# Kernel optimization log

Measured on AMD Instinct MI355X. Metric: run time of the kernel, lower is better.

The kernel has to match this reference:

```python
import jax, jax.numpy as jnp
import numpy as np

HIDDEN = 2048
N_HEADS = 16
N_KV = 4
HEAD_DIM = 128
EPS = 1e-6
B = 8
L = 1024
PREFIX = 256
SUFFIX = L - PREFIX
N_COMPACT = PREFIX + B * SUFFIX  # 6400
T_FULL = B * L                   # 8192
ROPE_THETA = 10000.0


def _radix_indices():
    # full position (b, p) -> compact index
    scatter = np.empty(T_FULL, dtype=np.int64)
    for b in range(B):
        scatter[b * L: b * L + PREFIX] = np.arange(PREFIX)
        scatter[b * L + PREFIX: (b + 1) * L] = PREFIX + b * SUFFIX + np.arange(SUFFIX)
    # compact index -> first full occurrence
    fold = np.empty(N_COMPACT, dtype=np.int64)
    fold[:PREFIX] = np.arange(PREFIX)
    for b in range(B):
        fold[PREFIX + b * SUFFIX: PREFIX + (b + 1) * SUFFIX] = b * L + PREFIX + np.arange(SUFFIX)
    return scatter, fold


def setup_inputs() -> dict:
    key = jax.random.key(0)
    ks = jax.random.split(key, 8)
    scatter_np, fold_np = _radix_indices()
    # per-compact-token positions for RoPE
    pos = np.empty(N_COMPACT, dtype=np.float32)
    pos[:PREFIX] = np.arange(PREFIX)
    for b in range(B):
        pos[PREFIX + b * SUFFIX: PREFIX + (b + 1) * SUFFIX] = PREFIX + np.arange(SUFFIX)
    inv_freq = ROPE_THETA ** (-np.arange(HEAD_DIM // 2, dtype=np.float32) / (HEAD_DIM // 2))
    freqs = pos[:, None] * inv_freq[None, :]  # [N_c, 64]
    s = 0.02
    return {
        "hidden_states": jax.random.normal(ks[0], (N_COMPACT, HIDDEN), jnp.float32),
        "cos": jnp.asarray(np.cos(freqs), jnp.float32),
        "sin": jnp.asarray(np.sin(freqs), jnp.float32),
        "cu_seq_lengths": jnp.arange(B + 1, dtype=jnp.int32) * L,
        "max_seq_len": L,
        "fold_gather": jnp.asarray(fold_np),
        "scatter_indices": jnp.asarray(scatter_np),
        "wq": jax.random.normal(ks[1], (HIDDEN, N_HEADS * HEAD_DIM), jnp.float32) * s,
        "wk": jax.random.normal(ks[2], (HIDDEN, N_KV * HEAD_DIM), jnp.float32) * s,
        "wv": jax.random.normal(ks[3], (HIDDEN, N_KV * HEAD_DIM), jnp.float32) * s,
        "wo": jax.random.normal(ks[4], (N_HEADS * HEAD_DIM, HIDDEN), jnp.float32) * s,
        "q_norm_w": jnp.ones((HEAD_DIM,), jnp.float32),
        "k_norm_w": jnp.ones((HEAD_DIM,), jnp.float32),
    }


def _rmsnorm(x, w):
    xf = x.astype(jnp.float32)
    var = jnp.mean(xf * xf, axis=-1, keepdims=True)
    return (w * (xf * jax.lax.rsqrt(var + EPS))).astype(x.dtype)


def _rope(x, cos, sin):
    # x: [N, H, D]; cos/sin: [N, D/2]
    half = cos.shape[-1]
    x1, x2 = x[..., :half], x[..., half:2 * half]
    c, s = cos[:, None, :], sin[:, None, :]
    return jnp.concatenate([x1 * c - x2 * s, x1 * s + x2 * c], axis=-1)


def reference(hidden_states, cos, sin, cu_seq_lengths, max_seq_len,
              fold_gather, scatter_indices, wq, wk, wv, wo, q_norm_w, k_norm_w):
    N = hidden_states.shape[0]
    q = (hidden_states @ wq).reshape(N, N_HEADS, HEAD_DIM)
    k = (hidden_states @ wk).reshape(N, N_KV, HEAD_DIM)
    v = (hidden_states @ wv).reshape(N, N_KV, HEAD_DIM)
    q = _rope(_rmsnorm(q, q_norm_w), cos, sin)
    k = _rope(_rmsnorm(k, k_norm_w), cos, sin)
    # radix scatter: expand compact tokens to full varlen token stream
    qf = q[scatter_indices].reshape(B, L, N_HEADS, HEAD_DIM)
    kf = k[scatter_indices].reshape(B, L, N_KV, HEAD_DIM)
    vf = v[scatter_indices].reshape(B, L, N_KV, HEAD_DIM)
    group = N_HEADS // N_KV
    kf = jnp.repeat(kf, group, axis=2)
    vf = jnp.repeat(vf, group, axis=2)
    scale = HEAD_DIM ** -0.5
    scores = jnp.einsum('bqhd,bkhd->bhqk', qf, kf) * scale
    causal = jnp.tril(jnp.ones((L, L), dtype=bool))
    scores = jnp.where(causal[None, None], scores, jnp.finfo(scores.dtype).min)
    probs = jax.nn.softmax(scores, axis=-1)
    out = jnp.einsum('bhqk,bkhd->bqhd', probs, vf).reshape(T_FULL, N_HEADS * HEAD_DIM)
    # radix fold: gather back to compact tokens
    out_compact = out[fold_gather]
    return out_compact @ wo
```

## Files before the change

### kernel.cpp

```cpp
#include <hip/hip_runtime.h>
#include <hip/hip_bf16.h>

typedef __bf16 bf16;
typedef __bf16 bf16x8 __attribute__((ext_vector_type(8)));
typedef float f32x4 __attribute__((ext_vector_type(4)));

#define HID 2048
#define NHEADS 16
#define NKV 4
#define HD 128
#define NC 6400
#define KVW (NKV * HD)

__device__ __forceinline__ void async_cp16(const bf16* src, bf16* dst_lds) {
  __builtin_amdgcn_global_load_lds(
      (const __attribute__((address_space(1))) void*)src,
      (__attribute__((address_space(3))) void*)dst_lds, 16, 0, 0);
}

__global__ __launch_bounds__(256) void k_cvt(const float* __restrict__ in,
                                             bf16* __restrict__ out) {
  size_t i = ((size_t)blockIdx.x * 256 + threadIdx.x) * 8;
  f32x4 a = *(const f32x4*)(in + i);
  f32x4 b = *(const f32x4*)(in + i + 4);
  bf16x8 t;
  for (int j = 0; j < 4; j++) {
    t[j] = (bf16)a[j];
    t[j + 4] = (bf16)b[j];
  }
  *(bf16x8*)(out + i) = t;
}

__global__ __launch_bounds__(256) void k_transpose(const float* __restrict__ in,
                                                   bf16* __restrict__ out,
                                                   int R, int C) {
  __shared__ bf16 tile[32][33];
  int bc = blockIdx.x * 32, br = blockIdx.y * 32;
  int tx = threadIdx.x & 31, ty = threadIdx.x >> 5;
  for (int i = 0; i < 32; i += 8)
    tile[ty + i][tx] = (bf16)in[(size_t)(br + ty + i) * C + bc + tx];
  __syncthreads();
  for (int i = 0; i < 32; i += 8)
    out[(size_t)(bc + ty + i) * R + br + tx] = tile[tx][ty + i];
}

__global__ __launch_bounds__(256) void k_proj(const bf16* __restrict__ A,
                                              const bf16* __restrict__ wqT,
                                              const bf16* __restrict__ wkT,
                                              const bf16* __restrict__ wvT,
                                              bf16* __restrict__ qb,
                                              bf16* __restrict__ kb,
                                              bf16* __restrict__ vtb) {
  __shared__ __align__(16) bf16 As[128][32];
  __shared__ __align__(16) bf16 Bs[128][32];
  const int K = HID;
  int n0 = blockIdx.x * 128, m0 = blockIdx.y * 128;
  int tid = threadIdx.x;
  int lane = tid & 63, wave = tid >> 6;
  int wm = (wave >> 1) * 64, wn = (wave & 1) * 64;
  int l15 = lane & 15, quad = lane >> 4;

  const bf16* bt;
  int nloc, outsel;
  if (n0 < HID) {
    bt = wqT; nloc = n0; outsel = 0;
  } else if (n0 < HID + KVW) {
    bt = wkT; nloc = n0 - HID; outsel = 1;
  } else {
    bt = wvT; nloc = n0 - HID - KVW; outsel = 2;
  }

  const f32x4 fz = {0.0f, 0.0f, 0.0f, 0.0f};
  f32x4 acc[4][4];
  for (int i = 0; i < 4; i++)
    for (int j = 0; j < 4; j++) acc[i][j] = fz;

  for (int k0 = 0; k0 < K; k0 += 32) {
    for (int s = 0; s < 2; s++) {
      int c = s * 256 + tid;
      int row = c >> 2, kc = c & 3;
      bf16* lbase = &As[0][0] + (size_t)(s * 256 + wave * 64) * 8;
      async_cp16(A + (size_t)(m0 + row) * K + k0 + kc * 8, lbase);
      bf16* lbase2 = &Bs[0][0] + (size_t)(s * 256 + wave * 64) * 8;
      async_cp16(bt + (size_t)(nloc + row) * K + k0 + kc * 8, lbase2);
    }
    __syncthreads();
    bf16x8 af[4], bfr[4];
    for (int t = 0; t < 4; t++) {
      af[t] = *(const bf16x8*)&As[wm + t * 16 + l15][quad * 8];
      bfr[t] = *(const bf16x8*)&Bs[wn + t * 16 + l15][quad * 8];
    }
    for (int i = 0; i < 4; i++)
      for (int j = 0; j < 4; j++)
        acc[i][j] =
            __builtin_amdgcn_mfma_f32_16x16x32_bf16(af[i], bfr[j], acc[i][j], 0, 0, 0);
    __syncthreads();
  }
  for (int i = 0; i < 4; i++)
    for (int j = 0; j < 4; j++)
      for (int r = 0; r < 4; r++) {
        int row = m0 + wm + i * 16 + quad * 4 + r;
        int col = nloc + wn + j * 16 + l15;
        float v = acc[i][j][r];
        if (outsel == 0)
          qb[(size_t)row * HID + col] = (bf16)v;
        else if (outsel == 1)
          kb[(size_t)row * KVW + col] = (bf16)v;
        else
          vtb[(size_t)col * NC + row] = (bf16)v;
      }
}

__global__ __launch_bounds__(256) void k_gemm_out(const bf16* __restrict__ A,
                                                  const bf16* __restrict__ Bt,
                                                  float* __restrict__ C,
                                                  int M, int N, int K) {
  __shared__ __align__(16) bf16 As[128][32];
  __shared__ __align__(16) bf16 Bs[128][32];
  int n0 = blockIdx.x * 128, m0 = blockIdx.y * 128;
  int tid = threadIdx.x;
  int lane = tid & 63, wave = tid >> 6;
  int wm = (wave >> 1) * 64, wn = (wave & 1) * 64;
  int l15 = lane & 15, quad = lane >> 4;

  const f32x4 fz = {0.0f, 0.0f, 0.0f, 0.0f};
  f32x4 acc[4][4];
  for (int i = 0; i < 4; i++)
    for (int j = 0; j < 4; j++) acc[i][j] = fz;

  for (int k0 = 0; k0 < K; k0 += 32) {
    for (int s = 0; s < 2; s++) {
      int c = s * 256 + tid;
      int row = c >> 2, kc = c & 3;
      bf16* lbase = &As[0][0] + (size_t)(s * 256 + wave * 64) * 8;
      async_cp16(A + (size_t)(m0 + row) * K + k0 + kc * 8, lbase);
      bf16* lbase2 = &Bs[0][0] + (size_t)(s * 256 + wave * 64) * 8;
      async_cp16(Bt + (size_t)(n0 + row) * K + k0 + kc * 8, lbase2);
    }
    __syncthreads();
    bf16x8 af[4], bfr[4];
    for (int t = 0; t < 4; t++) {
      af[t] = *(const bf16x8*)&As[wm + t * 16 + l15][quad * 8];
      bfr[t] = *(const bf16x8*)&Bs[wn + t * 16 + l15][quad * 8];
    }
    for (int i = 0; i < 4; i++)
      for (int j = 0; j < 4; j++)
        acc[i][j] =
            __builtin_amdgcn_mfma_f32_16x16x32_bf16(af[i], bfr[j], acc[i][j], 0, 0, 0);
    __syncthreads();
  }
  for (int i = 0; i < 4; i++)
    for (int j = 0; j < 4; j++)
      for (int r = 0; r < 4; r++) {
        int row = m0 + wm + i * 16 + quad * 4 + r;
        int col = n0 + wn + j * 16 + l15;
        C[(size_t)row * N + col] = acc[i][j][r];
      }
}

__global__ __launch_bounds__(256) void k_normrope(bf16* __restrict__ q,
                                                  bf16* __restrict__ k,
                                                  const float* __restrict__ cs,
                                                  const float* __restrict__ sn,
                                                  const float* __restrict__ qw,
                                                  const float* __restrict__ kw) {
  int pair = blockIdx.x * 4 + (threadIdx.x >> 6);
  int lane = threadIdx.x & 63;
  int n = pair / 20, hh = pair % 20;
  bf16* base;
  const float* w;
  if (hh < 16) {
    base = q + (size_t)n * HID + hh * HD;
    w = qw;
  } else {
    base = k + (size_t)n * KVW + (hh - 16) * HD;
    w = kw;
  }
  float x1 = (float)base[lane], x2 = (float)base[lane + 64];
  float ss = x1 * x1 + x2 * x2;
  for (int o = 32; o; o >>= 1) ss += __shfl_xor(ss, o);
  float inv = rsqrtf(ss * (1.0f / 128.0f) + 1e-6f);
  float x1n = x1 * inv * w[lane];
  float x2n = x2 * inv * w[lane + 64];
  float c = cs[(size_t)n * 64 + lane];
  float s = sn[(size_t)n * 64 + lane];
  base[lane] = (bf16)(x1n * c - x2n * s);
  base[lane + 64] = (bf16)(x1n * s + x2n * c);
}

__global__ __launch_bounds__(256) void k_attn(const bf16* __restrict__ qb,
                                              const bf16* __restrict__ kb,
                                              const bf16* __restrict__ vt,
                                              bf16* __restrict__ ob) {
  int qt = blockIdx.x;
  int h = blockIdx.y;
  int kh = h >> 2;
  int tid = threadIdx.x;
  int lane = tid & 63, wave = tid >> 6;
  int l15 = lane & 15, quad = lane >> 4;

  int b, p0, nbase;
  if (qt < 4) {
    b = 0;
    p0 = qt * 64;
    nbase = qt * 64;
  } else {
    int t = qt - 4;
    b = t / 12;
    int ti = t - b * 12;
    p0 = 256 + ti * 64;
    nbase = 256 + b * 768 + ti * 64;
  }

  __shared__ __align__(16) bf16 Ks[64][136];
  __shared__ __align__(16) bf16 Vs[128][72];
  __shared__ __align__(16) bf16 Ps[4][16][72];

  bf16x8 aq[4];
  {
    const bf16* qp =
        qb + (size_t)(nbase + wave * 16 + l15) * HID + h * HD + quad * 8;
    for (int ks = 0; ks < 4; ks++) aq[ks] = *(const bf16x8*)(qp + ks * 32);
  }
  int qpos[4];
  for (int r = 0; r < 4; r++) qpos[r] = p0 + wave * 16 + quad * 4 + r;

  const f32x4 fz = {0.0f, 0.0f, 0.0f, 0.0f};
  f32x4 oacc[8];
  for (int i = 0; i < 8; i++) oacc[i] = fz;
  float mrow[4], lrow[4];
  for (int r = 0; r < 4; r++) {
    mrow[r] = -3.0e38f;
    lrow[r] = 0.0f;
  }
  const float scale = 0.08838834764831845f;

  int nkt = p0 / 64 + 1;
  for (int kt = 0; kt < nkt; kt++) {
    int kpos0 = kt * 64;
    int kbase = (kpos0 < 256) ? kpos0 : 256 + b * 768 + (kpos0 - 256);
    __syncthreads();
    for (int s = 0; s < 4; s++) {
      int c = tid + 256 * s;
      int key = c >> 4, dc = c & 15;
      *(uint4*)&Ks[key][dc * 8] =
          *(const uint4*)(kb + (size_t)(kbase + key) * KVW + kh * HD + dc * 8);
    }
    for (int s = 0; s < 4; s++) {
      int c = tid + 256 * s;
      int d = c >> 3, kc = c & 7;
      *(uint4*)&Vs[d][kc * 8] =
          *(const uint4*)(vt + (size_t)(kh * HD + d) * NC + kbase + kc * 8);
    }
    __syncthreads();

    bool diag = (kt == nkt - 1);
    float sv[4][4];
    for (int nt = 0; nt < 4; nt++) {
      f32x4 z = fz;
      for (int ks = 0; ks < 4; ks++) {
        bf16x8 kf = *(const bf16x8*)&Ks[nt * 16 + l15][ks * 32 + quad * 8];
        z = __builtin_amdgcn_mfma_f32_16x16x32_bf16(aq[ks], kf, z, 0, 0, 0);
      }
      int kpos = kpos0 + nt * 16 + l15;
      for (int r = 0; r < 4; r++) {
        float v = z[r] * scale;
        if (diag && kpos > qpos[r]) v = -1.0e30f;
        sv[nt][r] = v;
      }
    }
    float alpha[4];
    for (int r = 0; r < 4; r++) {
      float mx = fmaxf(fmaxf(sv[0][r], sv[1][r]), fmaxf(sv[2][r], sv[3][r]));
      for (int o = 1; o < 16; o <<= 1) mx = fmaxf(mx, __shfl_xor(mx, o));
      float mnew = fmaxf(mrow[r], mx);
      alpha[r] = __expf(mrow[r] - mnew);
      mrow[r] = mnew;
      float ps = 0.0f;
      for (int nt = 0; nt < 4; nt++) {
        float p = __expf(sv[nt][r] - mnew);
        sv[nt][r] = p;
        ps += p;
      }
      for (int o = 1; o < 16; o <<= 1) ps += __shfl_xor(ps, o);
      lrow[r] = lrow[r] * alpha[r] + ps;
    }
    for (int i = 0; i < 8; i++)
      for (int r = 0; r < 4; r++) oacc[i][r] *= alpha[r];

    for (int nt = 0; nt < 4; nt++)
      for (int r = 0; r < 4; r++)
        Ps[wave][quad * 4 + r][nt * 16 + l15] = (bf16)sv[nt][r];
    __syncthreads();
    bf16x8 pa[2];
    for (int ks = 0; ks < 2; ks++)
      pa[ks] = *(const bf16x8*)&Ps[wave][l15][ks * 32 + quad * 8];
    for (int dt = 0; dt < 8; dt++)
      for (int ks = 0; ks < 2; ks++) {
        bf16x8 vf = *(const bf16x8*)&Vs[dt * 16 + l15][ks * 32 + quad * 8];
        oacc[dt] =
            __builtin_amdgcn_mfma_f32_16x16x32_bf16(pa[ks], vf, oacc[dt], 0, 0, 0);
      }
  }
  for (int r = 0; r < 4; r++) {
    float il = 1.0f / lrow[r];
    bf16* op = ob + (size_t)(nbase + wave * 16 + quad * 4 + r) * HID + h * HD;
    for (int dt = 0; dt < 8; dt++) op[dt * 16 + l15] = (bf16)(oacc[dt][r] * il);
  }
}

extern "C" void kernel_launch(void* const* d_in, const int* in_sizes, int n_in,
                              void* d_out, int out_size, void* d_ws,
                              size_t ws_size, hipStream_t stream) {
  const float* hs = (const float*)d_in[0];
  const float* cs = (const float*)d_in[1];
  const float* sn = (const float*)d_in[2];
  const float* wq = (const float*)d_in[7];
  const float* wk = (const float*)d_in[8];
  const float* wv = (const float*)d_in[9];
  const float* wo = (const float*)d_in[10];
  const float* qnw = (const float*)d_in[11];
  const float* knw = (const float*)d_in[12];
  float* out = (float*)d_out;

  bf16* hsb = (bf16*)d_out;
  bf16* wqT = hsb + (size_t)NC * HID;
  bf16* wkT = wqT + (size_t)HID * HID;
  bf16* wvT = wkT + (size_t)KVW * HID;
  bf16* qb  = (bf16*)d_in[0];
  bf16* ab  = qb + (size_t)NC * HID;
  bf16* woT = qb;
  bf16* kb  = (bf16*)d_ws;
  bf16* vtb = kb + (size_t)NC * KVW;

  k_cvt<<<dim3(NC * HID / (256 * 8)), 256, 0, stream>>>(hs, hsb);
  k_transpose<<<dim3(HID / 32, HID / 32), 256, 0, stream>>>(wq, wqT, HID, HID);
  k_transpose<<<dim3(KVW / 32, HID / 32), 256, 0, stream>>>(wk, wkT, HID, KVW);
  k_transpose<<<dim3(KVW / 32, HID / 32), 256, 0, stream>>>(wv, wvT, HID, KVW);

  k_proj<<<dim3((HID + 2 * KVW) / 128, NC / 128), 256, 0, stream>>>(
      hsb, wqT, wkT, wvT, qb, kb, vtb);

  k_normrope<<<dim3(NC * 20 / 4), 256, 0, stream>>>(qb, kb, cs, sn, qnw, knw);

  k_attn<<<dim3(100, NHEADS), 256, 0, stream>>>(qb, kb, vtb, ab);

  k_transpose<<<dim3(HID / 32, HID / 32), 256, 0, stream>>>(wo, woT, HID, HID);

  k_gemm_out<<<dim3(HID / 128, NC / 128), 256, 0, stream>>>(ab, woT, out, NC, HID, HID);
}
```

Before: 535.2 us.

## Rewrite projection GEMMs with 256x256 tiles, double-buffered swizzled LDS, and interleaved scheduling

Replaces the simple 128x128, K=32, single-buffer GEMM used for the QKV and output projections with a shared 256x256 tile core. The new core uses 512 threads, 64-wide K slabs, double-buffered LDS with an XOR swizzle, and async global-to-LDS loads interleaved with MFMA quarters under explicit waitcnt and barrier control. The aim is to hide memory latency, raise data reuse per tile and avoid LDS bank conflicts. In exchange it needs far more registers and LDS, which limits occupancy. The grid also shrinks to 25x12 and 25x8 blocks, which may leave some CUs underused, and the hand-written wait counts are fragile.

```diff
diff --git a/kernel.cpp b/kernel.cpp
--- a/kernel.cpp
+++ b/kernel.cpp
@@ -44,21 +44,160 @@
     out[(size_t)(bc + ty + i) * R + br + tx] = tile[tx][ty + i];
 }
 
-__global__ __launch_bounds__(256) void k_proj(const bf16* __restrict__ A,
-                                              const bf16* __restrict__ wqT,
-                                              const bf16* __restrict__ wkT,
-                                              const bf16* __restrict__ wvT,
-                                              bf16* __restrict__ qb,
-                                              bf16* __restrict__ kb,
-                                              bf16* __restrict__ vtb) {
-  __shared__ __align__(16) bf16 As[128][32];
-  __shared__ __align__(16) bf16 Bs[128][32];
-  const int K = HID;
-  int n0 = blockIdx.x * 128, m0 = blockIdx.y * 128;
-  int tid = threadIdx.x;
-  int lane = tid & 63, wave = tid >> 6;
-  int wm = (wave >> 1) * 64, wn = (wave & 1) * 64;
-  int l15 = lane & 15, quad = lane >> 4;
+__device__ __forceinline__ void gemm256_core(
+    const bf16* __restrict__ A, const bf16* __restrict__ Bt, int m0, int nloc,
+    int K, bf16* AsB, bf16* BsB, f32x4 (&acc)[2][4][4]) {
+  const int tid = threadIdx.x;
+  const int lane = tid & 63, wave = tid >> 6;
+  const int l15 = lane & 15, quad = lane >> 4;
+  const int wr = wave >> 2, wc = wave & 3;
+  const int r0A = wr * 128 + l15;
+  const int r0B = wc * 64 + l15;
+  const int colOff0 = (quad * 8) ^ ((l15 & 7) << 3);
+  const int colOff1 = (32 + quad * 8) ^ ((l15 & 7) << 3);
+  const int c0 = tid, c1 = 512 + tid;
+  const size_t offS0 =
+      (size_t)(c0 >> 3) * K + (((((c0 & 7) << 4) ^ (((c0 >> 3) & 7) << 4))) >> 1);
+  const size_t offS1 =
+      (size_t)(c1 >> 3) * K + (((((c1 & 7) << 4) ^ (((c1 >> 3) & 7) << 4))) >> 1);
+  const int dstW0 = wave * 512;
+  const int dstW1 = 4096 + wave * 512;
+  const bf16* Abase = A + (size_t)m0 * K;
+  const bf16* Bbase = Bt + (size_t)nloc * K;
+  const int KM = K - 1;
+
+#define STAGE(gb, lds, dbuf, h, kc)                             \
+  do {                                                          \
+    const bf16* _s = (gb) + (size_t)(h) * 128 * K + (kc);       \
+    bf16* _d = (lds) + (dbuf) * 16384 + (h) * 8192;             \
+    async_cp16(_s + offS0, _d + dstW0);                         \
+    async_cp16(_s + offS1, _d + dstW1);                         \
+  } while (0)
+
+#define LDA(dbuf, mh)                                           \
+  do {                                                          \
+    _Pragma("unroll") for (int i = 0; i < 4; i++) {             \
+      int r = r0A + (mh) * 64 + i * 16;                         \
+      const bf16* p = AsB + (dbuf) * 16384 + r * 64;            \
+      a[i][0] = *(const bf16x8*)(p + colOff0);                  \
+      a[i][1] = *(const bf16x8*)(p + colOff1);                  \
+    }                                                           \
+  } while (0)
+
+#define LDB(dbuf, nh, bb)                                       \
+  do {                                                          \
+    _Pragma("unroll") for (int j = 0; j < 2; j++) {             \
+      int r = r0B + (nh) * 32 + j * 16;                         \
+      const bf16* p = BsB + (dbuf) * 16384 + r * 64;            \
+      bb[j][0] = *(const bf16x8*)(p + colOff0);                 \
+      bb[j][1] = *(const bf16x8*)(p + colOff1);                 \
+    }                                                           \
+  } while (0)
+
+#define MFMAQ(mh, nh, bb)                                                    \
+  do {                                                                       \
+    __builtin_amdgcn_s_setprio(1);                                           \
+    _Pragma("unroll") for (int i = 0; i < 4; i++)                            \
+        _Pragma("unroll") for (int j = 0; j < 2; j++) {                      \
+      acc[mh][i][(nh) * 2 + j] = __builtin_amdgcn_mfma_f32_16x16x32_bf16(    \
+          a[i][0], bb[j][0], acc[mh][i][(nh) * 2 + j], 0, 0, 0);             \
+      acc[mh][i][(nh) * 2 + j] = __builtin_amdgcn_mfma_f32_16x16x32_bf16(    \
+          a[i][1], bb[j][1], acc[mh][i][(nh) * 2 + j], 0, 0, 0);             \
+    }                                                                        \
+    __builtin_amdgcn_s_setprio(0);                                           \
+  } while (0)
+
+  STAGE(Abase, AsB, 0, 0, 0);
+  STAGE(Abase, AsB, 0, 1, 0);
+  STAGE(Bbase, BsB, 0, 0, 0);
+  STAGE(Bbase, BsB, 0, 1, 0);
+  STAGE(Bbase, BsB, 1, 0, 64);
+  STAGE(Bbase, BsB, 1, 1, 64);
+  asm volatile("s_waitcnt vmcnt(4)" ::: "memory");
+  __builtin_amdgcn_s_barrier();
+  __builtin_amdgcn_sched_barrier(0);
+
+  bf16x8 a[4][2], b0[2][2], b1[2][2];
+
+  const int NIT = K >> 7;
+#pragma unroll 1
+  for (int it = 0; it < NIT; ++it) {
+    const int kb = it << 7;
+    LDA(0, 0);
+    LDB(0, 0, b0);
+    STAGE(Abase, AsB, 1, 0, (kb + 64) & KM);
+    asm volatile("s_waitcnt lgkmcnt(8)");
+    __builtin_amdgcn_s_barrier();
+    asm volatile("s_waitcnt lgkmcnt(0)" ::: "memory");
+    MFMAQ(0, 0, b0);
+    __builtin_amdgcn_s_barrier();
+    __builtin_amdgcn_sched_barrier(0);
+    LDB(0, 1, b1);
+    STAGE(Abase, AsB, 1, 1, (kb + 64) & KM);
+    __builtin_amdgcn_s_barrier();
+    asm volatile("s_waitcnt lgkmcnt(0)" ::: "memory");
+    MFMAQ(0, 1, b1);
+    __builtin_amdgcn_s_barrier();
+    __builtin_amdgcn_sched_barrier(0);
+    LDA(0, 1);
+    STAGE(Bbase, BsB, 0, 0, (kb + 128) & KM);
+    __builtin_amdgcn_s_barrier();
+    asm volatile("s_waitcnt lgkmcnt(0)" ::: "memory");
+    MFMAQ(1, 0, b0);
+    __builtin_amdgcn_s_barrier();
+    __builtin_amdgcn_sched_barrier(0);
+    STAGE(Bbase, BsB, 0, 1, (kb + 128) & KM);
+    __builtin_amdgcn_s_barrier();
+    MFMAQ(1, 1, b1);
+    asm volatile("s_waitcnt vmcnt(4)" ::: "memory");
+    __builtin_amdgcn_s_barrier();
+    __builtin_amdgcn_sched_barrier(0);
+    LDA(1, 0);
+    LDB(1, 0, b0);
+    STAGE(Abase, AsB, 0, 0, (kb + 128) & KM);
+    asm volatile("s_waitcnt lgkmcnt(8)");
+    __builtin_amdgcn_s_barrier();
+    asm volatile("s_waitcnt lgkmcnt(0)" ::: "memory");
+    MFMAQ(0, 0, b0);
+    __builtin_amdgcn_s_barrier();
+    __builtin_amdgcn_sched_barrier(0);
+    LDB(1, 1, b1);
+    STAGE(Abase, AsB, 0, 1, (kb + 128) & KM);
+    __builtin_amdgcn_s_barrier();
+    asm volatile("s_waitcnt lgkmcnt(0)" ::: "memory");
+    MFMAQ(0, 1, b1);
+    __builtin_amdgcn_s_barrier();
+    __builtin_amdgcn_sched_barrier(0);
+    LDA(1, 1);
+    STAGE(Bbase, BsB, 1, 0, (kb + 192) & KM);
+    __builtin_amdgcn_s_barrier();
+    asm volatile("s_waitcnt lgkmcnt(0)" ::: "memory");
+    MFMAQ(1, 0, b0);
+    __builtin_amdgcn_s_barrier();
+    __builtin_amdgcn_sched_barrier(0);
+    STAGE(Bbase, BsB, 1, 1, (kb + 192) & KM);
+    __builtin_amdgcn_s_barrier();
+    MFMAQ(1, 1, b1);
+    asm volatile("s_waitcnt vmcnt(4)" ::: "memory");
+    __builtin_amdgcn_s_barrier();
+    __builtin_amdgcn_sched_barrier(0);
+  }
+#undef STAGE
+#undef LDA
+#undef LDB
+#undef MFMAQ
+}
+
+__global__ __launch_bounds__(512, 2) void k_proj(const bf16* __restrict__ A,
+                                                 const bf16* __restrict__ wqT,
+                                                 const bf16* __restrict__ wkT,
+                                                 const bf16* __restrict__ wvT,
+                                                 bf16* __restrict__ qb,
+                                                 bf16* __restrict__ kb,
+                                                 bf16* __restrict__ vtb) {
+  __shared__ __align__(16) bf16 As[2][256][64];
+  __shared__ __align__(16) bf16 Bs[2][256][64];
+  int n0 = blockIdx.x * 256, m0 = blockIdx.y * 256;
 
   const bf16* bt;
   int nloc, outsel;
@@ -71,91 +210,73 @@
   }
 
   const f32x4 fz = {0.0f, 0.0f, 0.0f, 0.0f};
-  f32x4 acc[4][4];
-  for (int i = 0; i < 4; i++)
-    for (int j = 0; j < 4; j++) acc[i][j] = fz;
-
-  for (int k0 = 0; k0 < K; k0 += 32) {
-    for (int s = 0; s < 2; s++) {
-      int c = s * 256 + tid;
-      int row = c >> 2, kc = c & 3;
-      bf16* lbase = &As[0][0] + (size_t)(s * 256 + wave * 64) * 8;
-      async_cp16(A + (size_t)(m0 + row) * K + k0 + kc * 8, lbase);
-      bf16* lbase2 = &Bs[0][0] + (size_t)(s * 256 + wave * 64) * 8;
-      async_cp16(bt + (size_t)(nloc + row) * K + k0 + kc * 8, lbase2);
-    }
-    __syncthreads();
-    bf16x8 af[4], bfr[4];
-    for (int t = 0; t < 4; t++) {
-      af[t] = *(const bf16x8*)&As[wm + t * 16 + l15][quad * 8];
-      bfr[t] = *(const bf16x8*)&Bs[wn + t * 16 + l15][quad * 8];
-    }
+  f32x4 acc[2][4][4];
+#pragma unroll
+  for (int mh = 0; mh < 2; mh++)
+#pragma unroll
     for (int i = 0; i < 4; i++)
-      for (int j = 0; j < 4; j++)
-        acc[i][j] =
-            __builtin_amdgcn_mfma_f32_16x16x32_bf16(af[i], bfr[j], acc[i][j], 0, 0, 0);
-    __syncthreads();
-  }
-  for (int i = 0; i < 4; i++)
-    for (int j = 0; j < 4; j++)
-      for (int r = 0; r < 4; r++) {
-        int row = m0 + wm + i * 16 + quad * 4 + r;
-        int col = nloc + wn + j * 16 + l15;
-        float v = acc[i][j][r];
-        if (outsel == 0)
-          qb[(size_t)row * HID + col] = (bf16)v;
-        else if (outsel == 1)
-          kb[(size_t)row * KVW + col] = (bf16)v;
-        else
-          vtb[(size_t)col * NC + row] = (bf16)v;
-      }
-}
-
-__global__ __launch_bounds__(256) void k_gemm_out(const bf16* __restrict__ A,
-                                                  const bf16* __restrict__ Bt,
-                                                  float* __restrict__ C,
-                                                  int M, int N, int K) {
-  __shared__ __align__(16) bf16 As[128][32];
-  __shared__ __align__(16) bf16 Bs[128][32];
-  int n0 = blockIdx.x * 128, m0 = blockIdx.y * 128;
-  int tid = threadIdx.x;
-  int lane = tid & 63, wave = tid >> 6;
-  int wm = (wave >> 1) * 64, wn = (wave & 1) * 64;
+#pragma unroll
+      for (int j = 0; j < 4; j++) acc[mh][i][j] = fz;
+
+  gemm256_core(A, bt, m0, nloc, HID, &As[0][0][0], &Bs[0][0][0], acc);
+
+  int tid = threadIdx.x, lane = tid & 63, wave = tid >> 6;
   int l15 = lane & 15, quad = lane >> 4;
+  int wr = wave >> 2, wc = wave & 3;
+#pragma unroll
+  for (int mh = 0; mh < 2; mh++)
+#pragma unroll
+    for (int i = 0; i < 4; i++)
+#pragma unroll
+      for (int nj = 0; nj < 4; nj++)
+#pragma unroll
+        for (int r = 0; r < 4; r++) {
+          int row = m0 + wr * 128 + mh * 64 + i * 16 + quad * 4 + r;
+          int col = nloc + wc * 64 + nj * 16 + l15;
+          float v = acc[mh][i][nj][r];
+          if (outsel == 0)
+            qb[(size_t)row * HID + col] = (bf16)v;
+          else if (outsel == 1)
+            kb[(size_t)row * KVW + col] = (bf16)v;
+          else
+            vtb[(size_t)col * NC + row] = (bf16)v;
+        }
+}
+
+__global__ __launch_bounds__(512, 2) void k_gemm_out(const bf16* __restrict__ A,
+                                                     const bf16* __restrict__ Bt,
+                                                     float* __restrict__ C,
+                                                     int M, int N, int K) {
+  __shared__ __align__(16) bf16 As[2][256][64];
+  __shared__ __align__(16) bf16 Bs[2][256][64];
+  int n0 = blockIdx.x * 256, m0 = blockIdx.y * 256;
 
   const f32x4 fz = {0.0f, 0.0f, 0.0f, 0.0f};
-  f32x4 acc[4][4];
-  for (int i = 0; i < 4; i++)
-    for (int j = 0; j < 4; j++) acc[i][j] = fz;
-
-  for (int k0 = 0; k0 < K; k0 += 32) {
-    for (int s = 0; s < 2; s++) {
-      int c = s * 256 + tid;
-      int row = c >> 2, kc = c & 3;
-      bf16* lbase = &As[0][0] + (size_t)(s * 256 + wave * 64) * 8;
-      async_cp16(A + (size_t)(m0 + row) * K + k0 + kc * 8, lbase);
-      bf16* lbase2 = &Bs[0][0] + (size_t)(s * 256 + wave * 64) * 8;
-      async_cp16(Bt + (size_t)(n0 + row) * K + k0 + kc * 8, lbase2);
-    }
-    __syncthreads();
-    bf16x8 af[4], bfr[4];
-    for (int t = 0; t < 4; t++) {
-      af[t] = *(const bf16x8*)&As[wm + t * 16 + l15][quad * 8];
-      bfr[t] = *(const bf16x8*)&Bs[wn + t * 16 + l15][quad * 8];
-    }
+  f32x4 acc[2][4][4];
+#pragma unroll
+  for (int mh = 0; mh < 2; mh++)
+#pragma unroll
     for (int i = 0; i < 4; i++)
-      for (int j = 0; j < 4; j++)
-        acc[i][j] =
-            __builtin_amdgcn_mfma_f32_16x16x32_bf16(af[i], bfr[j], acc[i][j], 0, 0, 0);
-    __syncthreads();
-  }
-  for (int i = 0; i < 4; i++)
-    for (int j = 0; j < 4; j++)
-      for (int r = 0; r < 4; r++) {
-        int row = m0 + wm + i * 16 + quad * 4 + r;
-        int col = n0 + wn + j * 16 + l15;
-        C[(size_t)row * N + col] = acc[i][j][r];
-      }
+#pragma unroll
+      for (int j = 0; j < 4; j++) acc[mh][i][j] = fz;
+
+  gemm256_core(A, Bt, m0, n0, K, &As[0][0][0], &Bs[0][0][0], acc);
+
+  int tid = threadIdx.x, lane = tid & 63, wave = tid >> 6;
+  int l15 = lane & 15, quad = lane >> 4;
+  int wr = wave >> 2, wc = wave & 3;
+#pragma unroll
+  for (int mh = 0; mh < 2; mh++)
+#pragma unroll
+    for (int i = 0; i < 4; i++)
+#pragma unroll
+      for (int nj = 0; nj < 4; nj++)
+#pragma unroll
+        for (int r = 0; r < 4; r++) {
+          int row = m0 + wr * 128 + mh * 64 + i * 16 + quad * 4 + r;
+          int col = n0 + wc * 64 + nj * 16 + l15;
+          C[(size_t)row * N + col] = acc[mh][i][nj][r];
+        }
 }
 
 __global__ __launch_bounds__(256) void k_normrope(bf16* __restrict__ q,
@@ -338,7 +459,7 @@
   k_transpose<<<dim3(KVW / 32, HID / 32), 256, 0, stream>>>(wk, wkT, HID, KVW);
   k_transpose<<<dim3(KVW / 32, HID / 32), 256, 0, stream>>>(wv, wvT, HID, KVW);
 
-  k_proj<<<dim3((HID + 2 * KVW) / 128, NC / 128), 256, 0, stream>>>(
+  k_proj<<<dim3((HID + 2 * KVW) / 256, NC / 256), 512, 0, stream>>>(
       hsb, wqT, wkT, wvT, qb, kb, vtb);
 
   k_normrope<<<dim3(NC * 20 / 4), 256, 0, stream>>>(qb, kb, cs, sn, qnw, knw);
@@ -347,5 +468,5 @@
 
   k_transpose<<<dim3(HID / 32, HID / 32), 256, 0, stream>>>(wo, woT, HID, HID);
 
-  k_gemm_out<<<dim3(HID / 128, NC / 128), 256, 0, stream>>>(ab, woT, out, NC, HID, HID);
-}
+  k_gemm_out<<<dim3(HID / 256, NC / 256), 512, 0, stream>>>(ab, woT, out, NC, HID, HID);
+}
```

Measured after the change: 512.1 us. 1.05x faster.
